# Kernel tuning notes

Measured on AMD Instinct MI355X. Metric: run time of the kernel, lower is better.

## Reference

```python
import jax, jax.numpy as jnp
import numpy as np

H_SPLITS = [2, 3, 3]          # crpe_window {3:2, 5:3, 7:3}
K_SIZES = [3, 5, 7]
NUM_HEADS = 8
EPS = 1e-6


def dwconv(x, w, b, k):
    # x: (B,C,H,W), w: (C,1,k,k) depthwise, 'same' padding
    y = jax.lax.conv_general_dilated(
        x, w, (1, 1), [(k // 2, k // 2)] * 2,
        feature_group_count=x.shape[1],
        dimension_numbers=('NCHW', 'OIHW', 'NCHW'))
    return y + b[None, :, None, None]


def layernorm(x, g, b):
    m = jnp.mean(x, -1, keepdims=True)
    v = jnp.var(x, -1, keepdims=True)
    return (x - m) * jax.lax.rsqrt(v + EPS) * g + b


def conv_rel_pos_enc(q, v, ws, bs, H, W):
    # ConvRelPosEnc (MPViT style, no cls token): q * depthwise_conv(v)
    B, h, N, Ch = q.shape
    v_img = v.transpose(0, 1, 3, 2).reshape(B, h * Ch, H, W)  # B (h Ch) H W
    splits = np.cumsum([hs * Ch for hs in H_SPLITS])[:-1]
    parts = jnp.split(v_img, splits, axis=1)
    conv_v = jnp.concatenate(
        [dwconv(p, w, b, k) for p, w, b, k in zip(parts, ws, bs, K_SIZES)], axis=1)
    conv_v = conv_v.reshape(B, h, Ch, N).transpose(0, 1, 3, 2)
    return q * conv_v


def setup_inputs() -> dict:
    key = jax.random.key(0)
    B, H, W, C, nd, r, mr = 8, 64, 64, 320, 4, 2, 4
    h = NUM_HEADS
    N = H * W
    Ch = C // h
    hid = C // r
    ks = jax.random.split(key, 16)
    s = 0.02
    return {
        'x': jax.random.normal(ks[0], (B, N, C), jnp.float32),
        'domain_label': jax.nn.one_hot(jax.random.randint(ks[1], (B,), 0, nd), nd, dtype=jnp.float32),
        'cpe_w': jax.random.normal(ks[2], (C, 1, 3, 3), jnp.float32) * s,
        'cpe_b': jnp.zeros((C,), jnp.float32),
        'ln1_g': jnp.ones((C,), jnp.float32), 'ln1_b': jnp.zeros((C,), jnp.float32),
        'qkv_w': jax.random.normal(ks[3], (3 * C, C), jnp.float32) * s,
        'qkv_b': jnp.zeros((3 * C,), jnp.float32),
        'crpe_w3': jax.random.normal(ks[4], (2 * Ch, 1, 3, 3), jnp.float32) * s,
        'crpe_b3': jnp.zeros((2 * Ch,), jnp.float32),
        'crpe_w5': jax.random.normal(ks[5], (3 * Ch, 1, 5, 5), jnp.float32) * s,
        'crpe_b5': jnp.zeros((3 * Ch,), jnp.float32),
        'crpe_w7': jax.random.normal(ks[6], (3 * Ch, 1, 7, 7), jnp.float32) * s,
        'crpe_b7': jnp.zeros((3 * Ch,), jnp.float32),
        'dom_w1': jax.random.normal(ks[7], (hid, nd), jnp.float32) * s,
        'dom_b1': jnp.zeros((hid,), jnp.float32),
        'dom_w2': jax.random.normal(ks[8], (C, hid), jnp.float32) * s,
        'dom_b2': jnp.zeros((C,), jnp.float32),
        'proj_w': jax.random.normal(ks[9], (C, C), jnp.float32) * s,
        'proj_b': jnp.zeros((C,), jnp.float32),
        'ln2_g': jnp.ones((C,), jnp.float32), 'ln2_b': jnp.zeros((C,), jnp.float32),
        'mlp_w1': jax.random.normal(ks[10], (mr * C, C), jnp.float32) * s,
        'mlp_b1': jnp.zeros((mr * C,), jnp.float32),
        'mlp_w2': jax.random.normal(ks[11], (C, mr * C), jnp.float32) * s,
        'mlp_b2': jnp.zeros((C,), jnp.float32),
        'H': H, 'W': W,
    }


def reference(x, domain_label, cpe_w, cpe_b, ln1_g, ln1_b, qkv_w, qkv_b,
              crpe_w3, crpe_b3, crpe_w5, crpe_b5, crpe_w7, crpe_b7,
              dom_w1, dom_b1, dom_w2, dom_b2, proj_w, proj_b,
              ln2_g, ln2_b, mlp_w1, mlp_b1, mlp_w2, mlp_b2, H, W):
    B, N, C = x.shape
    h = NUM_HEADS
    Ch = C // h
    scale = Ch ** -0.5
    # ConvPosEnc: depthwise 3x3 conv + residual
    img = x.transpose(0, 2, 1).reshape(B, C, H, W)
    x = (dwconv(img, cpe_w, cpe_b, 3) + img).reshape(B, C, N).transpose(0, 2, 1)
    # FactorAtt_ConvRelPosEnc_Sup
    cur = layernorm(x, ln1_g, ln1_b)
    qkv = (cur @ qkv_w.T + qkv_b).reshape(B, N, 3, h, Ch).transpose(2, 0, 3, 1, 4)
    q, k, v = qkv[0], qkv[1], qkv[2]          # (B,h,N,Ch) each
    k_sm = jax.nn.softmax(k, axis=2)          # softmax over tokens
    kv = jnp.einsum('bhnk,bhnv->bhkv', k_sm, v)   # (B,h,Ch,Ch)
    fa = jnp.einsum('bhnk,bhkv->bhnv', q, kv)
    fa = scale * fa + conv_rel_pos_enc(
        q, v, (crpe_w3, crpe_w5, crpe_w7), (crpe_b3, crpe_b5, crpe_b7), H, W)
    # domain gate: MLP(one_hot) -> softmax over heads, broadcast over tokens
    d = jax.nn.relu(domain_label @ dom_w1.T + dom_b1) @ dom_w2.T + dom_b2  # (B,C)
    d = jax.nn.softmax(d.reshape(B, h, 1, Ch), axis=1)
    att = (d * fa).transpose(0, 2, 1, 3).reshape(B, N, C)
    x = x + (att @ proj_w.T + proj_b)
    # MLP (GELU, ratio 4)
    cur = layernorm(x, ln2_g, ln2_b)
    cur = jax.nn.gelu(cur @ mlp_w1.T + mlp_b1, approximate=False) @ mlp_w2.T + mlp_b2
    return x + cur
```

## Files before the change

kernel.cpp:

```cpp
#include <hip/hip_runtime.h>
#include <hip/hip_bf16.h>
#include <math.h>
#include <type_traits>

#define B_    8
#define Nn    4096
#define Cc    320
#define QS    1024
#define ATT_SCALE 0.15811388300841897f

typedef __attribute__((ext_vector_type(8))) short s8v;
typedef __attribute__((ext_vector_type(4))) float f4v;

__device__ __forceinline__ float bf2f(short u) {
    return __uint_as_float(((unsigned int)(unsigned short)u) << 16);
}
__device__ __forceinline__ short f2bf(float f) {
    return (short)__bfloat16_as_ushort(__float2bfloat16(f));
}
__device__ __forceinline__ float gelu_fast(float v) {
    float u = v * (0.7978845608f + 0.0356774081f * v * v);
    float e = __expf(2.f * u);
    float t = 1.f - 2.f / (e + 1.f);
    return 0.5f * v * (1.f + t);
}

typedef const __attribute__((address_space(1))) unsigned int* gp1_t;
typedef __attribute__((address_space(3))) unsigned int* lp3_t;
__device__ __forceinline__ void gload16(const void* g, void* l) {
    __builtin_amdgcn_global_load_lds((gp1_t)g, (lp3_t)l, 16, 0, 0);
}

__global__ void cvt_all(const float* __restrict__ s0, const float* __restrict__ s1,
                        const float* __restrict__ s2, const float* __restrict__ s3,
                        __hip_bfloat16* __restrict__ d) {
    int i = blockIdx.x * 256 + threadIdx.x;
    if (i >= 1351680) return;
    const float* s; int j, rows, K;
    if (i < 327680)      { s = s0; j = i;          rows = 960;  K = 320; }
    else if (i < 450560) { s = s1; j = i - 327680; rows = 320;  K = 320; }
    else if (i < 860160) { s = s2; j = i - 450560; rows = 1280; K = 320; }
    else                 { s = s3; j = i - 860160; rows = 320;  K = 1280; }
    float v = (j / K < rows) ? s[j] : 0.f;
    d[i] = __float2bfloat16(v);
}

__global__ void ln_kernel(const float* __restrict__ x, const float* __restrict__ g,
                          const float* __restrict__ bt, __hip_bfloat16* __restrict__ out) {
    int bn = blockIdx.x;
    int lane = threadIdx.x;
    const float* row = x + (size_t)bn * Cc;
    float v[5];
    float s = 0.f, s2 = 0.f;
    #pragma unroll
    for (int i = 0; i < 5; ++i) {
        v[i] = row[lane + 64 * i];
        s += v[i];
        s2 += v[i] * v[i];
    }
    #pragma unroll
    for (int off = 32; off > 0; off >>= 1) {
        s  += __shfl_down(s, off);
        s2 += __shfl_down(s2, off);
    }
    s  = __shfl(s, 0);
    s2 = __shfl(s2, 0);
    float mean = s * (1.f / 320.f);
    float var  = s2 * (1.f / 320.f) - mean * mean;
    float rstd = rsqrtf(var + 1e-6f);
    __hip_bfloat16* orow = out + (size_t)bn * Cc;
    #pragma unroll
    for (int i = 0; i < 5; ++i) {
        int c = lane + 64 * i;
        orow[c] = __float2bfloat16((v[i] - mean) * rstd * g[c] + bt[c]);
    }
}

template<int ACT, int RES, int WF32, int WBF16, int KT>
__global__ __launch_bounds__(256) void gemm_mfma(
        const __hip_bfloat16* __restrict__ A, const __hip_bfloat16* __restrict__ W,
        const float* __restrict__ bias, const float* __restrict__ res,
        float* __restrict__ outf, __hip_bfloat16* __restrict__ outb,
        int NS, int Nreal) {
    __shared__ __align__(16) short As[128 * 64];
    __shared__ __align__(16) short Bs[128 * 64];
    int tid = threadIdx.x;
    int m0 = blockIdx.x << 7;
    int n0 = blockIdx.y << 7;
    int w = tid >> 6, lane = tid & 63;
    int wr = w >> 1, wc = w & 1;
    int lrow = lane & 15, lk = lane >> 4;
    f4v acc[4][4];
    #pragma unroll
    for (int i = 0; i < 4; ++i)
        #pragma unroll
        for (int j = 0; j < 4; ++j) acc[i][j] = (f4v){0.f, 0.f, 0.f, 0.f};

    int srow = w * 32 + (lane >> 3);
    int slot = lane & 7;

    #pragma unroll
    for (int k0 = 0; k0 < KT; k0 += 64) {
        __syncthreads();
        #pragma unroll
        for (int i = 0; i < 4; ++i) {
            int row = srow + i * 8;
            int sk = (slot ^ (row & 7)) << 3;
            gload16(&A[(size_t)(m0 + row) * KT + k0 + sk], &As[w * 2048 + i * 512]);
            gload16(&W[(size_t)(n0 + row) * KT + k0 + sk], &Bs[w * 2048 + i * 512]);
        }
        __syncthreads();
        #pragma unroll
        for (int ks = 0; ks < 2; ++ks) {
            s8v af[4], bf[4];
            #pragma unroll
            for (int mi = 0; mi < 4; ++mi) {
                int row = wr * 64 + mi * 16 + lrow;
                int s = (ks * 4 + lk) ^ (row & 7);
                af[mi] = *reinterpret_cast<const s8v*>(&As[row * 64 + s * 8]);
            }
            #pragma unroll
            for (int ni = 0; ni < 4; ++ni) {
                int row = wc * 64 + ni * 16 + lrow;
                int s = (ks * 4 + lk) ^ (row & 7);
                bf[ni] = *reinterpret_cast<const s8v*>(&Bs[row * 64 + s * 8]);
            }
            #pragma unroll
            for (int mi = 0; mi < 4; ++mi)
                #pragma unroll
                for (int ni = 0; ni < 4; ++ni)
                    acc[mi][ni] = __builtin_amdgcn_mfma_f32_16x16x32_bf16(bf[ni], af[mi], acc[mi][ni], 0, 0, 0);
        }
    }

    #pragma unroll
    for (int mi = 0; mi < 4; ++mi) {
        int m = m0 + wr * 64 + mi * 16 + lrow;
        #pragma unroll
        for (int ni = 0; ni < 4; ++ni) {
            int n = n0 + wc * 64 + ni * 16 + (lk << 2);
            if (n >= Nreal) continue;
            f4v v4 = acc[mi][ni];
            float4 bv = *reinterpret_cast<const float4*>(&bias[n]);
            v4[0] += bv.x; v4[1] += bv.y; v4[2] += bv.z; v4[3] += bv.w;
            if (RES) {
                float4 rv = *reinterpret_cast<const float4*>(&res[(size_t)m * NS + n]);
                v4[0] += rv.x; v4[1] += rv.y; v4[2] += rv.z; v4[3] += rv.w;
            }
            if (ACT == 1) {
                #pragma unroll
                for (int r = 0; r < 4; ++r) v4[r] = gelu_fast(v4[r]);
            }
            if (WF32)
                *reinterpret_cast<float4*>(&outf[(size_t)m * NS + n]) =
                    make_float4(v4[0], v4[1], v4[2], v4[3]);
            if (WBF16) {
                ushort4 u;
                u.x = (unsigned short)f2bf(v4[0]);
                u.y = (unsigned short)f2bf(v4[1]);
                u.z = (unsigned short)f2bf(v4[2]);
                u.w = (unsigned short)f2bf(v4[3]);
                *reinterpret_cast<ushort4*>(&outb[(size_t)m * NS + n]) = u;
            }
        }
    }
}

template<int KSZ, int EPI, typename ST>
__global__ __launch_bounds__(256) void dwconv_tile(
        const ST* __restrict__ src, int sstride, int scoff,
        const float* __restrict__ wts, const float* __restrict__ bias, int cbase, int ngrp,
        const float* __restrict__ aux0,
        const float* __restrict__ aux1,
        float* __restrict__ outf, __hip_bfloat16* __restrict__ outb) {
    constexpr int P = KSZ / 2;
    constexpr int S = 16 + 2 * P;
    __shared__ float vt[S * S * 8];
    __shared__ float ws_[8 * KSZ * KSZ];
    int blk = blockIdx.x;
    int tile = blk & 15;
    int g  = (blk >> 4) % ngrp;
    int b  = (blk >> 4) / ngrp;
    int ty0 = (tile >> 2) << 4;
    int tx0 = (tile & 3) << 4;
    int c0 = cbase + g * 8;
    int tid = threadIdx.x;
    for (int e = tid; e < 8 * KSZ * KSZ; e += 256)
        ws_[e] = wts[g * 8 * KSZ * KSZ + e];
    const ST* sb = src + (size_t)b * Nn * sstride + scoff + c0;
    for (int e = tid; e < S * S; e += 256) {
        int hy = e / S, hx = e % S;
        int gy = ty0 - P + hy, gx = tx0 - P + hx;
        float px8[8];
        #pragma unroll
        for (int j = 0; j < 8; ++j) px8[j] = 0.f;
        if ((unsigned)gy < 64u && (unsigned)gx < 64u) {
            const ST* p = &sb[(size_t)((gy << 6) + gx) * sstride];
            if constexpr (std::is_same<ST, float>::value) {
                float4 lo = reinterpret_cast<const float4*>(p)[0];
                float4 hi = reinterpret_cast<const float4*>(p)[1];
                px8[0] = lo.x; px8[1] = lo.y; px8[2] = lo.z; px8[3] = lo.w;
                px8[4] = hi.x; px8[5] = hi.y; px8[6] = hi.z; px8[7] = hi.w;
            } else {
                s8v v8 = *reinterpret_cast<const s8v*>(p);
                #pragma unroll
                for (int j = 0; j < 8; ++j) px8[j] = bf2f(v8[j]);
            }
        }
        #pragma unroll
        for (int j = 0; j < 8; ++j) vt[e * 8 + j] = px8[j];
    }
    __syncthreads();
    int cl  = tid & 7;
    int px  = (tid >> 3) & 15;
    int pyh = tid >> 7;
    int c = c0 + cl;
    float acc[8];
    float bval = bias[g * 8 + cl];
    #pragma unroll
    for (int j = 0; j < 8; ++j) acc[j] = bval;
    #pragma unroll
    for (int dx = 0; dx < KSZ; ++dx) {
        float col[8 + KSZ - 1];
        #pragma unroll
        for (int i = 0; i < 8 + KSZ - 1; ++i)
            col[i] = vt[((pyh * 8 + i) * S + (px + dx)) * 8 + cl];
        #pragma unroll
        for (int j = 0; j < 8; ++j)
            #pragma unroll
            for (int dy = 0; dy < KSZ; ++dy)
                acc[j] += col[j + dy] * ws_[cl * KSZ * KSZ + dy * KSZ + dx];
    }
    #pragma unroll
    for (int j = 0; j < 8; ++j) {
        int n = ((ty0 + pyh * 8 + j) << 6) + tx0 + px;
        size_t bn = (size_t)b * Nn + n;
        if (EPI == 0) {
            outf[bn * Cc + c] = acc[j] + aux0[bn * Cc + c];
        } else {
            float qv  = bf2f(((const short*)src)[bn * (size_t)sstride + c]);
            float fav = aux0[bn * Cc + c];
            float r = aux1[(size_t)b * Cc + c] * (ATT_SCALE * fav + qv * acc[j]);
            outb[bn * Cc + c] = __float2bfloat16(r);
        }
    }
}

__global__ __launch_bounds__(256) void kv_mfma(const __hip_bfloat16* __restrict__ qkv,
                                               float* __restrict__ kvp) {
    __shared__ short lds[4 * 2 * 48 * 66];
    int blk = blockIdx.x;
    int s = blk & 7;
    int bh = blk >> 3;
    int h = bh & 7, b = bh >> 3;
    int tid = threadIdx.x;
    int w = tid >> 6, lane = tid & 63;
    short* ke_t = lds + w * 2 * 48 * 66;
    short* vv_t = ke_t + 48 * 66;
    for (int e = lane; e < 8 * 66; e += 64) {
        ke_t[40 * 66 + e] = 0;
        vv_t[40 * 66 + e] = 0;
    }
    for (int n = lane; n < 66; n += 64) vv_t[40 * 66 + n] = (short)0x3F80;

    const short* kb = (const short*)qkv + (size_t)b * Nn * QS + 320 + h * 40;
    const short* vb = kb + 320;
    int col0 = lane & 15, kq = lane >> 4;
    f4v acc[3][3];
    #pragma unroll
    for (int i = 0; i < 3; ++i)
        #pragma unroll
        for (int j = 0; j < 3; ++j) acc[i][j] = (f4v){0.f, 0.f, 0.f, 0.f};

    for (int t = w; t < 8; t += 4) {
        int n0 = s * 512 + t * 64;
        for (int e = lane; e < 320; e += 64) {
            int nl = e / 5, oct = e % 5;
            size_t go = (size_t)(n0 + nl) * QS + oct * 8;
            s8v k8 = *reinterpret_cast<const s8v*>(kb + go);
            s8v v8 = *reinterpret_cast<const s8v*>(vb + go);
            #pragma unroll
            for (int j = 0; j < 8; ++j) {
                ke_t[(oct * 8 + j) * 66 + nl] = f2bf(__expf(bf2f(k8[j])));
                vv_t[(oct * 8 + j) * 66 + nl] = v8[j];
            }
        }
        __syncthreads();
        #pragma unroll
        for (int ks = 0; ks < 2; ++ks) {
            s8v af[3], bfr[3];
            #pragma unroll
            for (int mt = 0; mt < 3; ++mt)
                af[mt] = *reinterpret_cast<const s8v*>(ke_t + (mt * 16 + col0) * 66 + ks * 32 + kq * 8);
            #pragma unroll
            for (int nt = 0; nt < 3; ++nt)
                bfr[nt] = *reinterpret_cast<const s8v*>(vv_t + (nt * 16 + col0) * 66 + ks * 32 + kq * 8);
            #pragma unroll
            for (int mt = 0; mt < 3; ++mt)
                #pragma unroll
                for (int nt = 0; nt < 3; ++nt)
                    acc[mt][nt] = __builtin_amdgcn_mfma_f32_16x16x32_bf16(af[mt], bfr[nt], acc[mt][nt], 0, 0, 0);
        }
        __syncthreads();
    }
    float* red = (float*)lds;
    #pragma unroll
    for (int mt = 0; mt < 3; ++mt) {
        #pragma unroll
        for (int nt = 0; nt < 3; ++nt) {
            #pragma unroll
            for (int r = 0; r < 4; ++r) {
                int ch = mt * 16 + kq * 4 + r;
                int cv = nt * 16 + col0;
                if (ch < 40) red[w * 1920 + ch * 48 + cv] = acc[mt][nt][r];
            }
        }
    }
    __syncthreads();
    for (int p = tid; p < 1920; p += 256) {
        float sv = red[p] + red[1920 + p] + red[2 * 1920 + p] + red[3 * 1920 + p];
        kvp[(size_t)blk * 1920 + p] = sv;
    }
}

__global__ void kv_combine2(const float* __restrict__ kvp, float* __restrict__ kv) {
    int bh = blockIdx.x;
    int tid = threadIdx.x;
    __shared__ float sinv[40];
    if (tid < 40) {
        float S = 0.f;
        for (int s2 = 0; s2 < 8; ++s2)
            S += kvp[(size_t)(bh * 8 + s2) * 1920 + tid * 48 + 40];
        sinv[tid] = 1.f / S;
    }
    __syncthreads();
    for (int p = tid; p < 1600; p += 256) {
        int ch = p / 40, cv = p % 40;
        float v = 0.f;
        for (int s2 = 0; s2 < 8; ++s2)
            v += kvp[(size_t)(bh * 8 + s2) * 1920 + ch * 48 + cv];
        kv[(size_t)bh * 1600 + p] = v * sinv[ch];
    }
}

__global__ void dgate_kernel(const float* __restrict__ lbl, const float* __restrict__ w1,
                             const float* __restrict__ b1, const float* __restrict__ w2,
                             const float* __restrict__ b2, float* __restrict__ dg) {
    int b = blockIdx.x;
    int tid = threadIdx.x;
    __shared__ float hid[160];
    __shared__ float dd[320];
    if (tid < 160) {
        float a = b1[tid];
        for (int d = 0; d < 4; ++d) a += w1[tid * 4 + d] * lbl[b * 4 + d];
        hid[tid] = fmaxf(a, 0.f);
    }
    __syncthreads();
    float a = b2[tid];
    for (int j = 0; j < 160; ++j) a += w2[tid * 160 + j] * hid[j];
    dd[tid] = a;
    __syncthreads();
    if (tid < 40) {
        float M = -1e30f;
        for (int h2 = 0; h2 < 8; ++h2) M = fmaxf(M, dd[h2 * 40 + tid]);
        float S = 0.f;
        float e[8];
        for (int h2 = 0; h2 < 8; ++h2) { e[h2] = __expf(dd[h2 * 40 + tid] - M); S += e[h2]; }
        float inv = 1.f / S;
        for (int h2 = 0; h2 < 8; ++h2) dg[b * 320 + h2 * 40 + tid] = e[h2] * inv;
    }
}

__global__ __launch_bounds__(256) void fa_kernel(const __hip_bfloat16* __restrict__ qkv,
        const float* __restrict__ kvmat, float* __restrict__ fa) {
    __shared__ float kvs[1600];
    int blk = blockIdx.x;
    int chunk = blk & 15;
    int bh = blk >> 4;
    int h = bh & 7, b = bh >> 3;
    int tid = threadIdx.x;
    for (int e = tid; e < 1600; e += 256) kvs[e] = kvmat[(size_t)bh * 1600 + e];
    __syncthreads();
    int n = chunk * 256 + tid;
    const short* qr = (const short*)qkv + (size_t)(b * Nn + n) * QS + h * 40;
    float q[40];
    #pragma unroll
    for (int i = 0; i < 5; ++i) {
        s8v v8 = reinterpret_cast<const s8v*>(qr)[i];
        #pragma unroll
        for (int j = 0; j < 8; ++j) q[i * 8 + j] = bf2f(v8[j]);
    }
    float o[40];
    #pragma unroll
    for (int cv = 0; cv < 40; ++cv) o[cv] = 0.f;
    #pragma unroll
    for (int ch = 0; ch < 40; ++ch) {
        float qv = q[ch];
        #pragma unroll
        for (int cv = 0; cv < 40; ++cv)
            o[cv] += qv * kvs[ch * 40 + cv];
    }
    float* fr = fa + (size_t)(b * Nn + n) * 320 + h * 40;
    #pragma unroll
    for (int i = 0; i < 10; ++i)
        reinterpret_cast<float4*>(fr)[i] = make_float4(o[i * 4], o[i * 4 + 1], o[i * 4 + 2], o[i * 4 + 3]);
}

extern "C" void kernel_launch(void* const* d_in, const int* in_sizes, int n_in,
                              void* d_out, int out_size, void* d_ws, size_t ws_size,
                              hipStream_t stream) {
    const float* x     = (const float*)d_in[0];
    const float* lbl   = (const float*)d_in[1];
    const float* cpe_w = (const float*)d_in[2];
    const float* cpe_b = (const float*)d_in[3];
    const float* ln1g  = (const float*)d_in[4];
    const float* ln1b  = (const float*)d_in[5];
    const float* qkv_w = (const float*)d_in[6];
    const float* qkv_b = (const float*)d_in[7];
    const float* w3    = (const float*)d_in[8];
    const float* b3    = (const float*)d_in[9];
    const float* w5    = (const float*)d_in[10];
    const float* b5    = (const float*)d_in[11];
    const float* w7    = (const float*)d_in[12];
    const float* b7    = (const float*)d_in[13];
    const float* dw1   = (const float*)d_in[14];
    const float* db1   = (const float*)d_in[15];
    const float* dw2   = (const float*)d_in[16];
    const float* db2   = (const float*)d_in[17];
    const float* pw    = (const float*)d_in[18];
    const float* pb    = (const float*)d_in[19];
    const float* ln2g  = (const float*)d_in[20];
    const float* ln2b  = (const float*)d_in[21];
    const float* m1w   = (const float*)d_in[22];
    const float* m1b   = (const float*)d_in[23];
    const float* m2w   = (const float*)d_in[24];
    const float* m2b   = (const float*)d_in[25];
    float* out = (float*)d_out;

    float* ws = (float*)d_ws;
    float* x1   = ws; ws += 10485760;
    __hip_bfloat16* qkvb = (__hip_bfloat16*)ws; ws += 16777216;
    float* fa   = ws; ws += 20971520;
    __hip_bfloat16* gelub = (__hip_bfloat16*)fa;
    __hip_bfloat16* bb1   = (__hip_bfloat16*)ws; ws += 5242880;
    __hip_bfloat16* wb    = (__hip_bfloat16*)ws; ws += 675840;
    float* kvp  = ws; ws += 983040;
    float* kv   = ws; ws += 102400;
    float* dg   = ws; ws += 2560;
    __hip_bfloat16* wbq  = wb;
    __hip_bfloat16* wbp  = wbq  + 1024 * 320;
    __hip_bfloat16* wbm1 = wbp  + 384 * 320;
    __hip_bfloat16* wbm2 = wbm1 + 1280 * 320;

    cvt_all<<<5280, 256, 0, stream>>>(qkv_w, pw, m1w, m2w, wb);
    dwconv_tile<3, 0, float><<<B_ * 40 * 16, 256, 0, stream>>>(
        x, 320, 0, cpe_w, cpe_b, 0, 40, x, nullptr, x1, nullptr);
    ln_kernel<<<B_ * Nn, 64, 0, stream>>>(x1, ln1g, ln1b, bb1);
    {
        dim3 g(256, 8);
        gemm_mfma<0, 0, 0, 1, 320><<<g, 256, 0, stream>>>(bb1, wbq, qkv_b, nullptr,
                                                          nullptr, qkvb, QS, 960);
    }
    kv_mfma<<<512, 256, 0, stream>>>(qkvb, kvp);
    kv_combine2<<<64, 256, 0, stream>>>(kvp, kv);
    dgate_kernel<<<B_, 320, 0, stream>>>(lbl, dw1, db1, dw2, db2, dg);
    fa_kernel<<<B_ * 8 * 16, 256, 0, stream>>>(qkvb, kv, fa);
    dwconv_tile<3, 1, __hip_bfloat16><<<B_ * 10 * 16, 256, 0, stream>>>(
        qkvb, QS, 640, w3, b3, 0, 10, fa, dg, nullptr, bb1);
    dwconv_tile<5, 1, __hip_bfloat16><<<B_ * 15 * 16, 256, 0, stream>>>(
        qkvb, QS, 640, w5, b5, 80, 15, fa, dg, nullptr, bb1);
    dwconv_tile<7, 1, __hip_bfloat16><<<B_ * 15 * 16, 256, 0, stream>>>(
        qkvb, QS, 640, w7, b7, 200, 15, fa, dg, nullptr, bb1);
    {
        dim3 g(256, 3);
        gemm_mfma<0, 1, 1, 0, 320><<<g, 256, 0, stream>>>(bb1, wbp, pb, x1,
                                                          out, nullptr, 320, 320);
    }
    ln_kernel<<<B_ * Nn, 64, 0, stream>>>(out, ln2g, ln2b, bb1);
    {
        dim3 g(256, 10);
        gemm_mfma<1, 0, 0, 1, 320><<<g, 256, 0, stream>>>(bb1, wbm1, m1b, nullptr,
                                                          nullptr, gelub, 1280, 1280);
    }
    {
        dim3 g(256, 3);
        gemm_mfma<0, 1, 1, 0, 1280><<<g, 256, 0, stream>>>(gelub, wbm2, m2b, out,
                                                           out, nullptr, 320, 320);
    }
}
```

Measured before the change: 345.5 us.

## Add A-panel-resident GEMM streaming weight chunks and store fa in bf16

```diff
diff --git a/kernel.cpp b/kernel.cpp
--- a/kernel.cpp
+++ b/kernel.cpp
@@ -73,6 +73,120 @@
     for (int i = 0; i < 5; ++i) {
         int c = lane + 64 * i;
         orow[c] = __float2bfloat16((v[i] - mean) * rstd * g[c] + bt[c]);
+    }
+}
+
+template<int ACT, int RES, int WF32, int WBF16, int NCHUNK>
+__global__ __launch_bounds__(512) void gemm_panel(
+        const __hip_bfloat16* __restrict__ A, const __hip_bfloat16* __restrict__ W,
+        const float* __restrict__ bias, const float* __restrict__ res,
+        float* __restrict__ outf, __hip_bfloat16* __restrict__ outb,
+        int NS, int Nreal) {
+    constexpr int KP = 320, KSTEPS = 5, AP = 328;
+    __shared__ __align__(16) short Apan[128 * AP];
+    __shared__ __align__(16) short Wbuf[2][128 * 64];
+    int tid = threadIdx.x;
+    int m0 = blockIdx.x << 7;
+    int w = tid >> 6, lane = tid & 63;
+    int wr = w & 3, wc = w >> 2;
+    int lrow = lane & 15, lk = lane >> 4;
+
+    #pragma unroll
+    for (int i = 0; i < 10; ++i) {
+        int c = tid + i * 512;
+        int row = c / 40, ko = (c % 40) * 8;
+        s8v v = *reinterpret_cast<const s8v*>(&A[(size_t)(m0 + row) * KP + ko]);
+        *reinterpret_cast<s8v*>(&Apan[row * AP + ko]) = v;
+    }
+    int prow = (w << 3) + (lane >> 3);
+    int pslot = lane & 7;
+    auto WPREF = [&](int buf, int nc, int kc) {
+        #pragma unroll
+        for (int i = 0; i < 2; ++i) {
+            int row = i * 64 + prow;
+            int sk = (pslot ^ (row & 7)) << 3;
+            gload16(&W[(size_t)(nc * 128 + row) * KP + kc * 64 + sk],
+                    &Wbuf[buf][i * 4096 + w * 512]);
+        }
+    };
+    WPREF(0, 0, 0);
+    __syncthreads();
+
+    int step = 0;
+    for (int nc = 0; nc < NCHUNK; ++nc) {
+        f4v acc[2][4];
+        #pragma unroll
+        for (int i = 0; i < 2; ++i)
+            #pragma unroll
+            for (int j = 0; j < 4; ++j) acc[i][j] = (f4v){0.f, 0.f, 0.f, 0.f};
+        #pragma unroll
+        for (int kc = 0; kc < KSTEPS; ++kc, ++step) {
+            int buf = step & 1;
+            if (step + 1 < NCHUNK * KSTEPS) {
+                int t = step + 1;
+                WPREF(buf ^ 1, t / KSTEPS, t % KSTEPS);
+                asm volatile("s_waitcnt vmcnt(2)" ::: "memory");
+            } else {
+                asm volatile("s_waitcnt vmcnt(0)" ::: "memory");
+            }
+            __builtin_amdgcn_sched_barrier(0);
+            __builtin_amdgcn_s_barrier();
+            #pragma unroll
+            for (int ks = 0; ks < 2; ++ks) {
+                s8v af[2], bf[4];
+                #pragma unroll
+                for (int mi = 0; mi < 2; ++mi) {
+                    int row = wr * 32 + mi * 16 + lrow;
+                    af[mi] = *reinterpret_cast<const s8v*>(
+                        &Apan[row * AP + kc * 64 + (ks * 4 + lk) * 8]);
+                }
+                #pragma unroll
+                for (int ni = 0; ni < 4; ++ni) {
+                    int row = wc * 64 + ni * 16 + lrow;
+                    int s = (ks * 4 + lk) ^ (row & 7);
+                    bf[ni] = *reinterpret_cast<const s8v*>(&Wbuf[buf][row * 64 + s * 8]);
+                }
+                #pragma unroll
+                for (int mi = 0; mi < 2; ++mi)
+                    #pragma unroll
+                    for (int ni = 0; ni < 4; ++ni)
+                        acc[mi][ni] = __builtin_amdgcn_mfma_f32_16x16x32_bf16(
+                            bf[ni], af[mi], acc[mi][ni], 0, 0, 0);
+            }
+            __builtin_amdgcn_s_barrier();
+        }
+        int n0c = nc * 128;
+        #pragma unroll
+        for (int mi = 0; mi < 2; ++mi) {
+            int m = m0 + wr * 32 + mi * 16 + lrow;
+            #pragma unroll
+            for (int ni = 0; ni < 4; ++ni) {
+                int n = n0c + wc * 64 + ni * 16 + (lk << 2);
+                if (n >= Nreal) continue;
+                f4v v4 = acc[mi][ni];
+                float4 bv = *reinterpret_cast<const float4*>(&bias[n]);
+                v4[0] += bv.x; v4[1] += bv.y; v4[2] += bv.z; v4[3] += bv.w;
+                if (RES) {
+                    float4 rv = *reinterpret_cast<const float4*>(&res[(size_t)m * NS + n]);
+                    v4[0] += rv.x; v4[1] += rv.y; v4[2] += rv.z; v4[3] += rv.w;
+                }
+                if (ACT == 1) {
+                    #pragma unroll
+                    for (int r = 0; r < 4; ++r) v4[r] = gelu_fast(v4[r]);
+                }
+                if (WF32)
+                    *reinterpret_cast<float4*>(&outf[(size_t)m * NS + n]) =
+                        make_float4(v4[0], v4[1], v4[2], v4[3]);
+                if (WBF16) {
+                    ushort4 u;
+                    u.x = (unsigned short)f2bf(v4[0]);
+                    u.y = (unsigned short)f2bf(v4[1]);
+                    u.z = (unsigned short)f2bf(v4[2]);
+                    u.w = (unsigned short)f2bf(v4[3]);
+                    *reinterpret_cast<ushort4*>(&outb[(size_t)m * NS + n]) = u;
+                }
+            }
+        }
     }
 }
 
@@ -132,7 +246,6 @@
                     acc[mi][ni] = __builtin_amdgcn_mfma_f32_16x16x32_bf16(bf[ni], af[mi], acc[mi][ni], 0, 0, 0);
         }
     }
-
     #pragma unroll
     for (int mi = 0; mi < 4; ++mi) {
         int m = m0 + wr * 64 + mi * 16 + lrow;
@@ -170,7 +283,7 @@
 __global__ __launch_bounds__(256) void dwconv_tile(
         const ST* __restrict__ src, int sstride, int scoff,
         const float* __restrict__ wts, const float* __restrict__ bias, int cbase, int ngrp,
-        const float* __restrict__ aux0,
+        const void* __restrict__ aux0v,
         const float* __restrict__ aux1,
         float* __restrict__ outf, __hip_bfloat16* __restrict__ outb) {
     constexpr int P = KSZ / 2;
@@ -236,10 +349,12 @@
         int n = ((ty0 + pyh * 8 + j) << 6) + tx0 + px;
         size_t bn = (size_t)b * Nn + n;
         if (EPI == 0) {
+            const float* aux0 = (const float*)aux0v;
             outf[bn * Cc + c] = acc[j] + aux0[bn * Cc + c];
         } else {
+            const short* aux0 = (const short*)aux0v;
             float qv  = bf2f(((const short*)src)[bn * (size_t)sstride + c]);
-            float fav = aux0[bn * Cc + c];
+            float fav = bf2f(aux0[bn * Cc + c]);
             float r = aux1[(size_t)b * Cc + c] * (ATT_SCALE * fav + qv * acc[j]);
             outb[bn * Cc + c] = __float2bfloat16(r);
         }
@@ -372,7 +487,7 @@
 }
 
 __global__ __launch_bounds__(256) void fa_kernel(const __hip_bfloat16* __restrict__ qkv,
-        const float* __restrict__ kvmat, float* __restrict__ fa) {
+        const float* __restrict__ kvmat, __hip_bfloat16* __restrict__ fa) {
     __shared__ float kvs[1600];
     int blk = blockIdx.x;
     int chunk = blk & 15;
@@ -400,10 +515,14 @@
         for (int cv = 0; cv < 40; ++cv)
             o[cv] += qv * kvs[ch * 40 + cv];
     }
-    float* fr = fa + (size_t)(b * Nn + n) * 320 + h * 40;
-    #pragma unroll
-    for (int i = 0; i < 10; ++i)
-        reinterpret_cast<float4*>(fr)[i] = make_float4(o[i * 4], o[i * 4 + 1], o[i * 4 + 2], o[i * 4 + 3]);
+    short* fr = (short*)fa + (size_t)(b * Nn + n) * 320 + h * 40;
+    #pragma unroll
+    for (int i = 0; i < 5; ++i) {
+        s8v u;
+        #pragma unroll
+        for (int j = 0; j < 8; ++j) u[j] = f2bf(o[i * 8 + j]);
+        *reinterpret_cast<s8v*>(fr + i * 8) = u;
+    }
 }
 
 extern "C" void kernel_launch(void* const* d_in, const int* in_sizes, int n_in,
@@ -440,8 +559,9 @@
     float* ws = (float*)d_ws;
     float* x1   = ws; ws += 10485760;
     __hip_bfloat16* qkvb = (__hip_bfloat16*)ws; ws += 16777216;
-    float* fa   = ws; ws += 20971520;
-    __hip_bfloat16* gelub = (__hip_bfloat16*)fa;
+    float* big  = ws; ws += 20971520;
+    __hip_bfloat16* gelub = (__hip_bfloat16*)big;
+    __hip_bfloat16* fab   = (__hip_bfloat16*)ws; ws += 5242880;
     __hip_bfloat16* bb1   = (__hip_bfloat16*)ws; ws += 5242880;
     __hip_bfloat16* wb    = (__hip_bfloat16*)ws; ws += 675840;
     float* kvp  = ws; ws += 983040;
@@ -456,32 +576,23 @@
     dwconv_tile<3, 0, float><<<B_ * 40 * 16, 256, 0, stream>>>(
         x, 320, 0, cpe_w, cpe_b, 0, 40, x, nullptr, x1, nullptr);
     ln_kernel<<<B_ * Nn, 64, 0, stream>>>(x1, ln1g, ln1b, bb1);
-    {
-        dim3 g(256, 8);
-        gemm_mfma<0, 0, 0, 1, 320><<<g, 256, 0, stream>>>(bb1, wbq, qkv_b, nullptr,
-                                                          nullptr, qkvb, QS, 960);
-    }
+    gemm_panel<0, 0, 0, 1, 8><<<256, 512, 0, stream>>>(bb1, wbq, qkv_b, nullptr,
+                                                       nullptr, qkvb, QS, 960);
     kv_mfma<<<512, 256, 0, stream>>>(qkvb, kvp);
     kv_combine2<<<64, 256, 0, stream>>>(kvp, kv);
     dgate_kernel<<<B_, 320, 0, stream>>>(lbl, dw1, db1, dw2, db2, dg);
-    fa_kernel<<<B_ * 8 * 16, 256, 0, stream>>>(qkvb, kv, fa);
+    fa_kernel<<<B_ * 8 * 16, 256, 0, stream>>>(qkvb, kv, fab);
     dwconv_tile<3, 1, __hip_bfloat16><<<B_ * 10 * 16, 256, 0, stream>>>(
-        qkvb, QS, 640, w3, b3, 0, 10, fa, dg, nullptr, bb1);
+        qkvb, QS, 640, w3, b3, 0, 10, fab, dg, nullptr, bb1);
     dwconv_tile<5, 1, __hip_bfloat16><<<B_ * 15 * 16, 256, 0, stream>>>(
-        qkvb, QS, 640, w5, b5, 80, 15, fa, dg, nullptr, bb1);
+        qkvb, QS, 640, w5, b5, 80, 15, fab, dg, nullptr, bb1);
     dwconv_tile<7, 1, __hip_bfloat16><<<B_ * 15 * 16, 256, 0, stream>>>(
-        qkvb, QS, 640, w7, b7, 200, 15, fa, dg, nullptr, bb1);
-    {
-        dim3 g(256, 3);
-        gemm_mfma<0, 1, 1, 0, 320><<<g, 256, 0, stream>>>(bb1, wbp, pb, x1,
-                                                          out, nullptr, 320, 320);
-    }
+        qkvb, QS, 640, w7, b7, 200, 15, fab, dg, nullptr, bb1);
+    gemm_panel<0, 1, 1, 0, 3><<<256, 512, 0, stream>>>(bb1, wbp, pb, x1,
+                                                       out, nullptr, 320, 320);
     ln_kernel<<<B_ * Nn, 64, 0, stream>>>(out, ln2g, ln2b, bb1);
-    {
-        dim3 g(256, 10);
-        gemm_mfma<1, 0, 0, 1, 320><<<g, 256, 0, stream>>>(bb1, wbm1, m1b, nullptr,
-                                                          nullptr, gelub, 1280, 1280);
-    }
+    gemm_panel<1, 0, 0, 1, 10><<<256, 512, 0, stream>>>(bb1, wbm1, m1b, nullptr,
+                                                        nullptr, gelub, 1280, 1280);
     {
         dim3 g(256, 3);
         gemm_mfma<0, 1, 1, 0, 1280><<<g, 256, 0, stream>>>(gelub, wbm2, m2b, out,
```

New measurement: 387.9 us. 12.2% more time.
